# Optimization experiments

Measured on AMD Instinct MI355X. Metric: run time of the kernel, lower is better.

Reference implementation:

```python
import jax, jax.numpy as jnp
import numpy as np

D = 192
HEADS = 4
HD = D // HEADS
R = 3  # correlation radius actually used in forward_level
NDISP = (2 * R + 1) ** 2  # 49
T = 3  # frames -> 2 consecutive pairs
ITERS = 4


def layer_norm(x, w, b, eps=1e-5):
    m = jnp.mean(x, axis=-1, keepdims=True)
    v = jnp.var(x, axis=-1, keepdims=True)
    return (x - m) / jnp.sqrt(v + eps) * w + b


def mha(x, in_w, in_b, out_w, out_b):
    # torch nn.MultiheadAttention, batch_first, self-attention
    B, N, _ = x.shape
    qkv = x @ in_w.T + in_b
    q, k, v = jnp.split(qkv, 3, axis=-1)
    q = q.reshape(B, N, HEADS, HD).transpose(0, 2, 1, 3) * (1.0 / float(np.sqrt(HD)))
    k = k.reshape(B, N, HEADS, HD).transpose(0, 2, 1, 3)
    v = v.reshape(B, N, HEADS, HD).transpose(0, 2, 1, 3)
    att = jax.nn.softmax(jnp.einsum('bhqd,bhkd->bhqk', q, k), axis=-1)
    y = jnp.einsum('bhqk,bhkd->bhqd', att, v).transpose(0, 2, 1, 3).reshape(B, N, D)
    return y @ out_w.T + out_b


def tblock(x, p):
    ln1w, ln1b, inw, inb, ow, ob, ln2w, ln2b, w1, b1, w2, b2 = p
    x = x + mha(layer_norm(x, ln1w, ln1b), inw, inb, ow, ob)
    h = layer_norm(x, ln2w, ln2b)
    h = jax.nn.gelu(h @ w1.T + b1, approximate=False) @ w2.T + b2
    return x + h


def local_corr(f1, f2):
    C = f1.shape[1]
    scale = 1.0 / float(np.sqrt(C))
    outs = []
    for dy in range(-R, R + 1):
        for dx in range(-R, R + 1):
            f2s = jnp.roll(f2, (dy, dx), axis=(2, 3))
            outs.append(jnp.sum(f1 * f2s, axis=1) * scale)
    return jnp.stack(outs, axis=1)


def grid_sample_bilinear_border(img, grid):
    # img: B,C,H,W; grid: B,Ho,Wo,2 with (x,y) in [-1,1]; align_corners=True, border padding
    B, C, H, W = img.shape
    x = jnp.clip((grid[..., 0] + 1.0) * 0.5 * (W - 1), 0.0, W - 1)
    y = jnp.clip((grid[..., 1] + 1.0) * 0.5 * (H - 1), 0.0, H - 1)
    x0 = jnp.floor(x); y0 = jnp.floor(y)
    x1 = jnp.minimum(x0 + 1, W - 1); y1 = jnp.minimum(y0 + 1, H - 1)
    wx = (x - x0)[:, None]; wy = (y - y0)[:, None]
    imgf = img.reshape(B, C, H * W)
    Ho, Wo = x.shape[1], x.shape[2]
    def gather(yy, xx):
        idx = (yy * W + xx).astype(jnp.int32).reshape(B, 1, Ho * Wo)
        return jnp.take_along_axis(imgf, idx, axis=2).reshape(B, C, Ho, Wo)
    v00 = gather(y0, x0); v01 = gather(y0, x1)
    v10 = gather(y1, x0); v11 = gather(y1, x1)
    return v00 * (1 - wx) * (1 - wy) + v01 * wx * (1 - wy) + v10 * (1 - wx) * wy + v11 * wx * wy


def warp(img, flow):
    # flow in pixels, Bx2xHxW
    B, C, H, W = img.shape
    xs = jnp.linspace(-1.0, 1.0, W); ys = jnp.linspace(-1.0, 1.0, H)
    gx, gy = jnp.meshgrid(xs, ys)  # each (H, W), 'xy' indexing
    base = jnp.stack([gx, gy], axis=-1)[None]
    off = jnp.stack([flow[:, 0] * (2.0 / max(W - 1, 1)),
                     flow[:, 1] * (2.0 / max(H - 1, 1))], axis=-1)
    return grid_sample_bilinear_border(img, base + off)


def upsample2x_align(img):
    # F.interpolate(scale_factor=2, mode='bilinear', align_corners=True)
    B, C, H, W = img.shape
    Ho, Wo = 2 * H, 2 * W
    xs = jnp.linspace(-1.0, 1.0, Wo); ys = jnp.linspace(-1.0, 1.0, Ho)
    gx, gy = jnp.meshgrid(xs, ys)
    grid = jnp.broadcast_to(jnp.stack([gx, gy], axis=-1)[None], (B, Ho, Wo, 2))
    return grid_sample_bilinear_border(img, grid)


def conv2d(x, w, b):
    y = jax.lax.conv_general_dilated(x, w, (1, 1), ((1, 1), (1, 1)),
                                     dimension_numbers=('NCHW', 'OIHW', 'NCHW'))
    return y + b[None, :, None, None]


def _forward(feats_l1, feats_l2, feats_l3, tok_w, tok_b,
             lcm_ln1_w, lcm_ln1_b, lcm_in_w, lcm_in_b, lcm_out_w, lcm_out_b,
             lcm_ln2_w, lcm_ln2_b, lcm_mlp_w1, lcm_mlp_b1, lcm_mlp_w2, lcm_mlp_b2,
             gtr_ln1_w, gtr_ln1_b, gtr_in_w, gtr_in_b, gtr_out_w, gtr_out_b,
             gtr_ln2_w, gtr_ln2_b, gtr_mlp_w1, gtr_mlp_b1, gtr_mlp_w2, gtr_mlp_b2,
             head_w1, head_b1, head_w2, head_b2,
             ref1_w1, ref1_b1, ref1_w2, ref1_b2,
             ref0_w1, ref0_b1, ref0_w2, ref0_b2):
    feats = [[feats_l1[t] for t in range(T)],
             [feats_l2[t] for t in range(T)],
             [feats_l3[t] for t in range(T)]]
    # ---- CostTokenizer ----
    tokens = []
    for lvl in range(3):
        toks = []
        for k in range(T - 1):
            corr = local_corr(feats[lvl][k], feats[lvl][k + 1])
            toks.append(jnp.einsum('bchw,dc->bdhw', corr, tok_w[lvl]) + tok_b[lvl][None, :, None, None])
        tokens.append(toks)
    lcm_p = [(lcm_ln1_w[i], lcm_ln1_b[i], lcm_in_w[i], lcm_in_b[i], lcm_out_w[i], lcm_out_b[i],
              lcm_ln2_w[i], lcm_ln2_b[i], lcm_mlp_w1[i], lcm_mlp_b1[i], lcm_mlp_w2[i], lcm_mlp_b2[i])
             for i in range(lcm_ln1_w.shape[0])]
    gtr_p = [(gtr_ln1_w[i], gtr_ln1_b[i], gtr_in_w[i], gtr_in_b[i], gtr_out_w[i], gtr_out_b[i],
              gtr_ln2_w[i], gtr_ln2_b[i], gtr_mlp_w1[i], gtr_mlp_b1[i], gtr_mlp_w2[i], gtr_mlp_b2[i])
             for i in range(gtr_ln1_w.shape[0])]
    # ---- LatentCostMemory (EMA state; .detach() -> stop_gradient; state resets when N changes) ----
    state = None
    latent = []
    for toks in tokens:
        lvl_lat = []
        for tok in toks:
            B_, Dd, H, W = tok.shape
            x = tok.reshape(B_, Dd, H * W).transpose(0, 2, 1)  # b (h w) d
            for p in lcm_p:
                x = tblock(x, p)
            if state is None or state.shape[1] != x.shape[1]:
                state = jax.lax.stop_gradient(x)
            x = 0.8 * x + 0.2 * state
            state = jax.lax.stop_gradient(x)
            lvl_lat.append(x.transpose(0, 2, 1))  # b d n
        latent.append(lvl_lat)
    H8, W8 = feats[1][0].shape[-2:]
    coarse = []
    for lat in latent[1]:
        x = lat.transpose(0, 2, 1)
        for p in gtr_p:
            x = tblock(x, p)
        fv = jax.nn.gelu(x @ head_w1.T + head_b1, approximate=False) @ head_w2.T + head_b2
        coarse.append(fv.transpose(0, 2, 1).reshape(-1, 2, H8, W8))
    # ---- MSRecurrentDecoder ----
    outs = []
    for k, f8 in enumerate(coarse):
        cur = f8
        for _ in range(ITERS):
            w10 = warp(feats[1][k + 1], cur)
            x = jnp.concatenate([feats[1][k], cur, w10], axis=1)
            cur = cur + conv2d(jax.nn.gelu(conv2d(x, ref1_w1, ref1_b1), approximate=False), ref1_w2, ref1_b2)
        cur2 = upsample2x_align(cur)
        for _ in range(ITERS):
            w10 = warp(feats[0][k + 1], cur2)
            x = jnp.concatenate([feats[0][k], cur2, w10], axis=1)
            cur2 = cur2 + conv2d(jax.nn.gelu(conv2d(x, ref0_w1, ref0_b1), approximate=False), ref0_w2, ref0_b2)
        outs.append(cur2)
    return jnp.stack(outs)  # [pairs, B, 2, H/4, W/4]


def setup_inputs():
    key = jax.random.key(0)
    ks = iter(jax.random.split(key, 64))
    def rn(shape, s=1.0):
        return jax.random.normal(next(ks), shape, dtype=jnp.float32) * s
    B = 1
    inp = {}
    inp['feats_l1'] = rn((T, B, 64, 64, 64))
    inp['feats_l2'] = rn((T, B, 128, 32, 32))
    inp['feats_l3'] = rn((T, B, 192, 16, 16))
    inp['tok_w'] = rn((3, D, NDISP), 0.02)
    inp['tok_b'] = rn((3, D), 0.02)
    for pre, n in (('lcm', 6), ('gtr', 2)):
        inp[pre + '_ln1_w'] = jnp.ones((n, D), jnp.float32)
        inp[pre + '_ln1_b'] = jnp.zeros((n, D), jnp.float32)
        inp[pre + '_in_w'] = rn((n, 3 * D, D), 0.02)
        inp[pre + '_in_b'] = rn((n, 3 * D), 0.02)
        inp[pre + '_out_w'] = rn((n, D, D), 0.02)
        inp[pre + '_out_b'] = rn((n, D), 0.02)
        inp[pre + '_ln2_w'] = jnp.ones((n, D), jnp.float32)
        inp[pre + '_ln2_b'] = jnp.zeros((n, D), jnp.float32)
        inp[pre + '_mlp_w1'] = rn((n, 4 * D, D), 0.02)
        inp[pre + '_mlp_b1'] = rn((n, 4 * D), 0.02)
        inp[pre + '_mlp_w2'] = rn((n, D, 4 * D), 0.02)
        inp[pre + '_mlp_b2'] = rn((n, D), 0.02)
    inp['head_w1'] = rn((D, D), 0.02); inp['head_b1'] = rn((D,), 0.02)
    inp['head_w2'] = rn((2, D), 0.02); inp['head_b2'] = rn((2,), 0.02)
    inp['ref1_w1'] = rn((128, 258, 3, 3), 0.02); inp['ref1_b1'] = rn((128,), 0.02)
    inp['ref1_w2'] = rn((2, 128, 3, 3), 0.02); inp['ref1_b2'] = rn((2,), 0.02)
    inp['ref0_w1'] = rn((64, 130, 3, 3), 0.02); inp['ref0_b1'] = rn((64,), 0.02)
    inp['ref0_w2'] = rn((2, 64, 3, 3), 0.02); inp['ref0_b2'] = rn((2,), 0.02)
    return inp


def reference(feats_l1, feats_l2, feats_l3, tok_w, tok_b,
              lcm_ln1_w, lcm_ln1_b, lcm_in_w, lcm_in_b, lcm_out_w, lcm_out_b,
              lcm_ln2_w, lcm_ln2_b, lcm_mlp_w1, lcm_mlp_b1, lcm_mlp_w2, lcm_mlp_b2,
              gtr_ln1_w, gtr_ln1_b, gtr_in_w, gtr_in_b, gtr_out_w, gtr_out_b,
              gtr_ln2_w, gtr_ln2_b, gtr_mlp_w1, gtr_mlp_b1, gtr_mlp_w2, gtr_mlp_b2,
              head_w1, head_b1, head_w2, head_b2,
              ref1_w1, ref1_b1, ref1_w2, ref1_b2,
              ref0_w1, ref0_b1, ref0_w2, ref0_b2):
    return _forward(feats_l1, feats_l2, feats_l3, tok_w, tok_b,
                    lcm_ln1_w, lcm_ln1_b, lcm_in_w, lcm_in_b, lcm_out_w, lcm_out_b,
                    lcm_ln2_w, lcm_ln2_b, lcm_mlp_w1, lcm_mlp_b1, lcm_mlp_w2, lcm_mlp_b2,
                    gtr_ln1_w, gtr_ln1_b, gtr_in_w, gtr_in_b, gtr_out_w, gtr_out_b,
                    gtr_ln2_w, gtr_ln2_b, gtr_mlp_w1, gtr_mlp_b1, gtr_mlp_w2, gtr_mlp_b2,
                    head_w1, head_b1, head_w2, head_b2,
                    ref1_w1, ref1_b1, ref1_w2, ref1_b2,
                    ref0_w1, ref0_b1, ref0_w2, ref0_b2)
```

## Files before the change

kernel.cpp:

```cpp
#include <hip/hip_runtime.h>
#include <hip/hip_bf16.h>

typedef __hip_bfloat16 bf16;
typedef short bf16x8 __attribute__((ext_vector_type(8)));
typedef float f32x4 __attribute__((ext_vector_type(4)));

#define DEV __device__ __forceinline__

DEV float bf2f(bf16 v) { return __bfloat162float(v); }
DEV bf16 f2bf(float v) { return __float2bfloat16(v); }
DEV unsigned short bfr(float f) {
  bf16 h = __float2bfloat16(f);
  return *reinterpret_cast<unsigned short*>(&h);
}
DEV float shf(unsigned short u) {
  unsigned int x = ((unsigned int)u) << 16;
  return *reinterpret_cast<float*>(&x);
}
DEV float gelu_exact(float x) { return 0.5f * x * (1.0f + erff(x * 0.70710678118654752f)); }

DEV float ldw(const void* p, long i, int isb) {
  return isb ? __bfloat162float(((const bf16*)p)[i]) : ((const float*)p)[i];
}

__global__ void k_detect(const unsigned short* __restrict__ u, int* __restrict__ flag) {
  __shared__ int bad;
  if (threadIdx.x == 0) bad = 0;
  __syncthreads();
  for (int i = threadIdx.x; i < 8192; i += 256) {
    int expo = (u[i] >> 7) & 0xFF;
    if (expo >= 138) atomicOr(&bad, 1);
  }
  __syncthreads();
  if (threadIdx.x == 0) *flag = bad ? 0 : 1;
}
__global__ void k_setone(int* p) { *p = 1; }

__global__ void k_cvt(const void* __restrict__ s, float* __restrict__ d, int n,
                      const int* __restrict__ fl) {
  int isb = *fl;
  int i = blockIdx.x * blockDim.x + threadIdx.x;
  if (i < n) d[i] = ldw(s, i, isb);
}

__global__ void k_zerosh(unsigned short* __restrict__ p, int n8) {
  int i = blockIdx.x * blockDim.x + threadIdx.x;
  if (i < n8) { uint4 z = {0, 0, 0, 0}; *(uint4*)(p + (long)i * 8) = z; }
}

__global__ void k_padtokw(const void* __restrict__ tw, bf16* __restrict__ dst,
                          const int* __restrict__ fl) {
  int isb = *fl;
  int i = blockIdx.x * blockDim.x + threadIdx.x;
  if (i >= 12288) return;
  int n = i >> 6, k = i & 63;
  float v = (k < 49) ? ldw(tw, 9408 + (long)n * 49 + k, isb) : 0.0f;
  dst[i] = f2bf(v);
}

__global__ void k_packw(const void* __restrict__ src, bf16* __restrict__ dst,
                        int OC, int C, int ICT, int NP, int ICP, int n,
                        const int* __restrict__ fl) {
  int isb = *fl;
  int i = blockIdx.x * blockDim.x + threadIdx.x;
  if (i >= n) return;
  int s = i / (NP * ICP);
  int r = i - s * NP * ICP;
  int oc = r / ICP, icp = r - oc * ICP;
  float v = 0.0f;
  if (oc < OC) {
    int ic = -1;
    if (icp < C) ic = icp;
    else if (icp < 2 * C) ic = icp - C + C + 2;
    else if (icp < 2 * C + 2) ic = icp - 2 * C + C;
    if (ic >= 0 && ic < ICT) v = ldw(src, ((long)oc * ICT + ic) * 9 + s, isb);
  }
  dst[i] = f2bf(v);
}

__global__ void k_trans_feats(const void* __restrict__ in, bf16* __restrict__ Fp,
                              int F, int C, int HW, const int* __restrict__ fl) {
  int isb = *fl;
  int cpg = C >> 3;
  int n = F * HW * cpg;
  int i = blockIdx.x * blockDim.x + threadIdx.x;
  if (i >= n) return;
  int p = i % HW;
  int rem = i / HW;
  int c8 = rem % cpg;
  int f = rem / cpg;
  long base = (long)f * C * HW + (long)(c8 * 8) * HW + p;
  union { unsigned short u[8]; uint4 v; } pk;
#pragma unroll
  for (int j = 0; j < 8; ++j) pk.u[j] = bfr(ldw(in, base + (long)j * HW, isb));
  *(uint4*)((unsigned short*)Fp + ((long)f * HW + p) * C + c8 * 8) = pk.v;
}

template <int C, int ICP, int NP, int WW, int LGW>
__global__ __launch_bounds__(64) void k_conv1w(
    const bf16* __restrict__ Fp, const float* __restrict__ flow,
    const bf16* __restrict__ Wp, const float* __restrict__ bias,
    bf16* __restrict__ out) {
  constexpr int HH = WW, HW = WW * WW;
  constexpr int ACW = 18, APX = 54;
  constexpr int NK = ICP / 32;
  __shared__ unsigned short As[APX][40];
  __shared__ unsigned short Ws[144][40];
  __shared__ int pofs[APX];
  __shared__ int doff[APX][4];
  __shared__ float dwt[APX][4];
  __shared__ float ffl[APX][2];
  int ln = threadIdx.x;
  int quad = ln >> 4, l16 = ln & 15;
  int n0 = blockIdx.x * 16, m0 = blockIdx.y * 16, b = blockIdx.z;
  int py0 = m0 >> LGW, px0 = m0 & (WW - 1);
  const unsigned short* fcur = (const unsigned short*)Fp + (long)b * HW * C;
  const unsigned short* fnxt = (const unsigned short*)Fp + (long)(b + 1) * HW * C;
  const float* fl = flow + (long)b * 2 * HW;
  if (ln < APX) {
    int sr = ln / ACW, sc = ln - sr * ACW;
    int py = py0 + sr - 1, px = px0 + sc - 1;
    bool in = py >= 0 && py < HH && px >= 0 && px < WW;
    int p = in ? (py * WW + px) : 0;
    pofs[ln] = in ? p * C : -1;
    float fx = in ? fl[p] : 0.0f, fy = in ? fl[HW + p] : 0.0f;
    float x = fminf(fmaxf((float)px + fx, 0.0f), (float)(WW - 1));
    float y = fminf(fmaxf((float)py + fy, 0.0f), (float)(HH - 1));
    int x0 = (int)floorf(x), y0 = (int)floorf(y);
    int x1 = min(x0 + 1, WW - 1), y1 = min(y0 + 1, HH - 1);
    float wx = x - (float)x0, wy = y - (float)y0;
    dwt[ln][0] = in ? (1 - wx) * (1 - wy) : 0.0f;
    dwt[ln][1] = in ? wx * (1 - wy) : 0.0f;
    dwt[ln][2] = in ? (1 - wx) * wy : 0.0f;
    dwt[ln][3] = in ? wx * wy : 0.0f;
    doff[ln][0] = (y0 * WW + x0) * C; doff[ln][1] = (y0 * WW + x1) * C;
    doff[ln][2] = (y1 * WW + x0) * C; doff[ln][3] = (y1 * WW + x1) * C;
    ffl[ln][0] = in ? fx : 0.0f; ffl[ln][1] = in ? fy : 0.0f;
  }
  uint4 wrg[9];
  uint4 arg[4];
  uint4 qrg[4][4];
  auto ldW = [&](int kc) {
#pragma unroll
    for (int j = 0; j < 9; ++j) {
      int idx = ln + j * 64;
      int r = idx >> 2, c4 = idx & 3;
      int s = r >> 4, nl = r & 15;
      wrg[j] = *(const uint4*)((const unsigned short*)Wp +
               ((long)s * NP + n0 + nl) * ICP + kc * 32 + c4 * 8);
    }
  };
  auto stW = [&]() {
#pragma unroll
    for (int j = 0; j < 9; ++j) {
      int idx = ln + j * 64;
      int r = idx >> 2, c4 = idx & 3;
      *(uint4*)&Ws[r][c4 * 8] = wrg[j];
    }
  };
  auto ldA = [&](int kc) {
    int chb = kc * 32;
    if (chb < C) {
#pragma unroll
      for (int j = 0; j < 4; ++j) {
        int idx = ln + j * 64;
        if (idx < APX * 4) {
          int ap = idx >> 2, c4 = idx & 3;
          int po = pofs[ap];
          uint4 z = {0, 0, 0, 0};
          arg[j] = (po >= 0) ? *(const uint4*)(fcur + po + chb + c4 * 8) : z;
        }
      }
    } else if (chb < 2 * C) {
#pragma unroll
      for (int j = 0; j < 4; ++j) {
        int idx = ln + j * 64;
        if (idx < APX * 4) {
          int ap = idx >> 2, c4 = idx & 3;
          int c = chb - C + c4 * 8;
#pragma unroll
          for (int e = 0; e < 4; ++e)
            qrg[j][e] = *(const uint4*)(fnxt + doff[ap][e] + c);
        }
      }
    }
  };
  auto stA = [&](int kc) {
    int chb = kc * 32;
    if (chb < C) {
#pragma unroll
      for (int j = 0; j < 4; ++j) {
        int idx = ln + j * 64;
        if (idx < APX * 4) {
          int ap = idx >> 2, c4 = idx & 3;
          *(uint4*)&As[ap][c4 * 8] = arg[j];
        }
      }
    } else if (chb < 2 * C) {
#pragma unroll
      for (int j = 0; j < 4; ++j) {
        int idx = ln + j * 64;
        if (idx < APX * 4) {
          int ap = idx >> 2, c4 = idx & 3;
          union { unsigned short u[8]; uint4 v; } a0 = {.v = qrg[j][0]}, a1 = {.v = qrg[j][1]},
                                                  a2 = {.v = qrg[j][2]}, a3 = {.v = qrg[j][3]}, o;
          float q0 = dwt[ap][0], q1 = dwt[ap][1], q2 = dwt[ap][2], q3 = dwt[ap][3];
#pragma unroll
          for (int e = 0; e < 8; ++e)
            o.u[e] = bfr(shf(a0.u[e]) * q0 + shf(a1.u[e]) * q1 +
                         shf(a2.u[e]) * q2 + shf(a3.u[e]) * q3);
          *(uint4*)&As[ap][c4 * 8] = o.v;
        }
      }
    } else {
#pragma unroll
      for (int j = 0; j < 4; ++j) {
        int idx = ln + j * 64;
        if (idx < APX * 4) {
          int ap = idx >> 2, c4 = idx & 3;
          union { unsigned short u[8]; uint4 v; } o = { .v = {0, 0, 0, 0} };
          if (c4 == 0) { o.u[0] = bfr(ffl[ap][0]); o.u[1] = bfr(ffl[ap][1]); }
          *(uint4*)&As[ap][c4 * 8] = o.v;
        }
      }
    }
  };
  f32x4 ac0 = {}, ac1 = {}, ac2 = {};
  auto mm = [&]() {
#pragma unroll
    for (int s = 0; s < 9; ++s) {
      int ky = s / 3, kx = s - ky * 3;
      bf16x8 af = *(const bf16x8*)&As[ky * ACW + l16 + kx][quad * 8];
      bf16x8 wf = *(const bf16x8*)&Ws[s * 16 + l16][quad * 8];
      if (s % 3 == 0)      ac0 = __builtin_amdgcn_mfma_f32_16x16x32_bf16(af, wf, ac0, 0, 0, 0);
      else if (s % 3 == 1) ac1 = __builtin_amdgcn_mfma_f32_16x16x32_bf16(af, wf, ac1, 0, 0, 0);
      else                 ac2 = __builtin_amdgcn_mfma_f32_16x16x32_bf16(af, wf, ac2, 0, 0, 0);
    }
  };
  ldW(0); ldA(0);
  stW(); stA(0);
#pragma unroll
  for (int kc = 0; kc < NK; ++kc) {
    if (kc + 1 < NK) { ldW(kc + 1); ldA(kc + 1); }
    mm();
    if (kc + 1 < NK) { stW(); stA(kc + 1); }
  }
  int n = n0 + l16;
  float bv = bias[n];
  long rowbase = (long)b * (HH + 2) * (WW + 2) + (long)(py0 + 1) * (WW + 2);
#pragma unroll
  for (int r = 0; r < 4; ++r) {
    int px = px0 + quad * 4 + r;
    float v = gelu_exact(ac0[r] + ac1[r] + ac2[r] + bv);
    ((unsigned short*)out)[(rowbase + px + 1) * NP + n] = bfr(v);
  }
}

template <int C, int WW, int LGW>
__global__ __launch_bounds__(256) void k_conv2_dot(
    const bf16* __restrict__ mid, const bf16* __restrict__ Wq,
    const float* __restrict__ bias, float* __restrict__ cur) {
  constexpr int HH = WW;
  constexpr int HW = HH * WW;
  constexpr int Wp2 = WW + 2;
  constexpr int CPL = C / 64;
  int tid = threadIdx.x, wv = tid >> 6, ln = tid & 63;
  int gw = blockIdx.x * 4 + wv;
  int b = gw >> (2 * LGW);
  int p = gw & (HW - 1);
  int py = p >> LGW, px = p & (WW - 1);
  float r0 = cur[((long)b * 2 + 0) * HW + p];
  float r1 = cur[((long)b * 2 + 1) * HW + p];
  float b0 = bias[0], b1 = bias[1];
  const unsigned short* base = (const unsigned short*)mid +
      ((long)b * (HH + 2) * Wp2 + (long)py * Wp2 + px) * C + ln * CPL;
  const unsigned short* wb = (const unsigned short*)Wq + ln * CPL;
  float s0 = 0.0f, s1 = 0.0f;
#pragma unroll
  for (int t = 0; t < 9; ++t) {
    int dy = t / 3, dx = t - dy * 3;
    const unsigned short* ar = base + ((long)dy * Wp2 + dx) * C;
    const unsigned short* w0r = wb + (long)(t * 16 + 0) * C;
    const unsigned short* w1r = wb + (long)(t * 16 + 1) * C;
    if (CPL == 2) {
      unsigned int a = *(const unsigned int*)ar;
      unsigned int q0 = *(const unsigned int*)w0r;
      unsigned int q1 = *(const unsigned int*)w1r;
      float a0 = shf((unsigned short)a), a1 = shf((unsigned short)(a >> 16));
      s0 += a0 * shf((unsigned short)q0) + a1 * shf((unsigned short)(q0 >> 16));
      s1 += a0 * shf((unsigned short)q1) + a1 * shf((unsigned short)(q1 >> 16));
    } else {
      float a0 = shf(ar[0]);
      s0 += a0 * shf(w0r[0]);
      s1 += a0 * shf(w1r[0]);
    }
  }
#pragma unroll
  for (int o = 32; o; o >>= 1) { s0 += __shfl_xor(s0, o); s1 += __shfl_xor(s1, o); }
  if (ln == 0) {
    cur[((long)b * 2 + 0) * HW + p] = s0 + b0 + r0;
    cur[((long)b * 2 + 1) * HW + p] = s1 + b1 + r1;
  }
}

__global__ void k_corr(const bf16* __restrict__ Fp2, bf16* __restrict__ corrT) {
  __shared__ unsigned short f1r[128];
  int p = blockIdx.x;
  int b = blockIdx.y;
  int t = threadIdx.x;
  const unsigned short* f1 = (const unsigned short*)Fp2 + ((long)b * 1024 + p) * 128;
  if (t < 16) *(uint4*)&f1r[t * 8] = *(const uint4*)(f1 + t * 8);
  __syncthreads();
  long rowo = ((long)b * 1024 + p) * 64;
  if (t < 49) {
    int dy = t / 7 - 3, dx = t % 7 - 3;
    int h = p >> 5, w = p & 31;
    int p2 = (((h - dy) & 31) << 5) | ((w - dx) & 31);
    const unsigned short* f2 = (const unsigned short*)Fp2 + ((long)(b + 1) * 1024 + p2) * 128;
    float s = 0.0f;
    for (int c = 0; c < 128; c += 8) {
      union { unsigned short u[8]; uint4 v; } av = { .v = *(const uint4*)&f1r[c] };
      union { unsigned short u[8]; uint4 v; } bv = { .v = *(const uint4*)(f2 + c) };
#pragma unroll
      for (int j = 0; j < 8; ++j) s += shf(av.u[j]) * shf(bv.u[j]);
    }
    corrT[rowo + t] = f2bf(s * 0.08838834764831845f);
  } else {
    corrT[rowo + t] = f2bf(0.0f);
  }
}

template <int KT, int BM, int ACT, bool HASRES, int AMODE, int OUTBF, int VT>
__global__ __launch_bounds__(256) void k_gemm_mfma2(
    const void* __restrict__ A, const void* __restrict__ W, long woff,
    const void* __restrict__ bias, long boff, const int* __restrict__ flb,
    const float* __restrict__ res, void* __restrict__ C,
    int M, int N, const int* __restrict__ fl,
    const unsigned short* __restrict__ mop, const float* __restrict__ mml,
    bf16* __restrict__ vtout,
    const void* __restrict__ lnw, long lnwoff,
    const void* __restrict__ lnb, long lnboff) {
  (void)M;
  int isb = *fl;
  constexpr int NKC = ((KT < 192) ? KT : 192) >> 5;
  constexpr int WM = (BM == 64) ? 4 : 2;
  constexpr int NTW = (BM == 64) ? 4 : 2;
  constexpr int LPR = 256 / BM;
  constexpr int EPL = 192 / LPR;
  __shared__ unsigned short Asm[NKC][BM][40];
  __shared__ unsigned short Wsm[NKC][64][40];
  int tid = threadIdx.x;
  int wv = tid >> 6, ln = tid & 63;
  int quad = ln >> 4, l16 = ln & 15;
  int wm = wv % WM, wn = wv / WM;
  int m0 = blockIdx.y * BM, n0 = blockIdx.x * 64;
  f32x4 acc[NTW] = {};
  for (int s0 = 0; s0 < KT; s0 += 192) {
    if (s0) __syncthreads();
    for (int i = tid; i < NKC * 256; i += 256) {
      int c4 = i & 3, r = (i >> 2) & 63, kc = i >> 8;
      long eo = woff + (long)(n0 + r) * KT + s0 + kc * 32 + c4 * 8;
      if (isb) {
        *(uint4*)&Wsm[kc][r][c4 * 8] = *(const uint4*)((const unsigned short*)W + eo);
      } else {
        const float* wp = (const float*)W + eo;
        float4 w0 = *(const float4*)wp;
        float4 w1 = *(const float4*)(wp + 4);
        union { unsigned short u[8]; uint4 v; } pk;
        pk.u[0] = bfr(w0.x); pk.u[1] = bfr(w0.y); pk.u[2] = bfr(w0.z); pk.u[3] = bfr(w0.w);
        pk.u[4] = bfr(w1.x); pk.u[5] = bfr(w1.y); pk.u[6] = bfr(w1.z); pk.u[7] = bfr(w1.w);
        *(uint4*)&Wsm[kc][r][c4 * 8] = pk.v;
      }
    }
    if constexpr (AMODE == 1) {
      for (int i = tid; i < NKC * BM * 4; i += 256) {
        int c4 = i & 3, r = (i >> 2) % BM, kc = i / (BM * 4);
        const unsigned short* ap =
            (const unsigned short*)A + (long)(m0 + r) * KT + s0 + kc * 32 + c4 * 8;
        *(uint4*)&Asm[kc][r][c4 * 8] = *(const uint4*)ap;
      }
    } else if constexpr (AMODE == 0) {
      for (int i = tid; i < NKC * BM * 4; i += 256) {
        int c4 = i & 3, r = (i >> 2) % BM, kc = i / (BM * 4);
        const float* ap = (const float*)A + (long)(m0 + r) * KT + s0 + kc * 32 + c4 * 8;
        float4 a0 = *(const float4*)ap;
        float4 a1 = *(const float4*)(ap + 4);
        union { unsigned short u[8]; uint4 v; } pk;
        pk.u[0] = bfr(a0.x); pk.u[1] = bfr(a0.y); pk.u[2] = bfr(a0.z); pk.u[3] = bfr(a0.w);
        pk.u[4] = bfr(a1.x); pk.u[5] = bfr(a1.y); pk.u[6] = bfr(a1.z); pk.u[7] = bfr(a1.w);
        *(uint4*)&Asm[kc][r][c4 * 8] = pk.v;
      }
    } else if constexpr (AMODE == 3) {
      int row = tid / LPR, j = tid % LPR;
      const float* xr = (const float*)A + (long)(m0 + row) * 192 + j * EPL;
      float av[EPL];
#pragma unroll
      for (int q4 = 0; q4 < EPL / 4; ++q4) {
        float4 v = *(const float4*)(xr + q4 * 4);
        av[q4 * 4 + 0] = v.x; av[q4 * 4 + 1] = v.y;
        av[q4 * 4 + 2] = v.z; av[q4 * 4 + 3] = v.w;
      }
      float sum = 0.0f;
#pragma unroll
      for (int q = 0; q < EPL; ++q) sum += av[q];
#pragma unroll
      for (int o = 1; o < LPR; o <<= 1) sum += __shfl_xor(sum, o);
      float mean = sum * (1.0f / 192.0f);
      float vs = 0.0f;
#pragma unroll
      for (int q = 0; q < EPL; ++q) { float d = av[q] - mean; vs += d * d; }
#pragma unroll
      for (int o = 1; o < LPR; o <<= 1) vs += __shfl_xor(vs, o);
      float rstd = rsqrtf(vs * (1.0f / 192.0f) + 1e-5f);
#pragma unroll
      for (int g = 0; g < EPL / 8; ++g) {
        int k = j * EPL + g * 8;
        union { unsigned short u[8]; uint4 v; } pk;
#pragma unroll
        for (int e = 0; e < 8; ++e) {
          float gg = ldw(lnw, lnwoff + k + e, isb);
          float bb = ldw(lnb, lnboff + k + e, isb);
          pk.u[e] = bfr((av[g * 8 + e] - mean) * rstd * gg + bb);
        }
        *(uint4*)&Asm[k >> 5][row][k & 31] = pk.v;
      }
    } else {
      int row = tid / LPR, j = tid % LPR;
      int m = m0 + row;
      int rr = m & 1023, bb = m >> 10;
#pragma unroll
      for (int g = 0; g < EPL / 8; ++g) {
        int k = j * EPL + g * 8;
        int h = k / 48;
        int d0 = k - h * 48;
        long idx[4];
        float ms[4], ls[4];
        float Ms = -1e30f;
#pragma unroll
        for (int s = 0; s < 4; ++s) {
          idx[s] = (((long)s * 2 + bb) * 4 + h) * 1024 + rr;
          ms[s] = mml[idx[s] * 2];
          ls[s] = mml[idx[s] * 2 + 1];
          Ms = fmaxf(Ms, ms[s]);
        }
        float e[4], L = 0.0f;
#pragma unroll
        for (int s = 0; s < 4; ++s) { e[s] = __expf(ms[s] - Ms); L += ls[s] * e[s]; }
        float invL = 1.0f / L;
        union { unsigned short u[8]; uint4 v; } pk;
#pragma unroll
        for (int e2 = 0; e2 < 8; ++e2) {
          float o = 0.0f;
#pragma unroll
          for (int s = 0; s < 4; ++s) o += shf(mop[idx[s] * 48 + d0 + e2]) * e[s];
          pk.u[e2] = bfr(o * invL);
        }
        *(uint4*)&Asm[k >> 5][row][k & 31] = pk.v;
      }
    }
    __syncthreads();
#pragma unroll
    for (int kc = 0; kc < NKC; ++kc) {
      bf16x8 af = *(const bf16x8*)&Asm[kc][wm * 16 + l16][quad * 8];
#pragma unroll
      for (int nt = 0; nt < NTW; ++nt) {
        bf16x8 wf = *(const bf16x8*)&Wsm[kc][(wn * NTW + nt) * 16 + l16][quad * 8];
        acc[nt] = __builtin_amdgcn_mfma_f32_16x16x32_bf16(af, wf, acc[nt], 0, 0, 0);
      }
    }
  }
  int isbb = *flb;
#pragma unroll
  for (int nt = 0; nt < NTW; ++nt) {
    int n = n0 + (wn * NTW + nt) * 16 + l16;
    float bv = ldw(bias, boff + n, isbb);
#pragma unroll
    for (int r = 0; r < 4; ++r) {
      int m = m0 + wm * 16 + quad * 4 + r;
      float v = acc[nt][r] + bv;
      if (HASRES) v += res[(long)m * N + n];
      if (ACT == 1) v = gelu_exact(v);
      if (OUTBF) ((bf16*)C)[(long)m * N + n] = f2bf(v);
      else ((float*)C)[(long)m * N + n] = v;
      if constexpr (VT) {
        if (n >= 384) {
          int hh = (n - 384) / 48, dd = (n - 384) % 48;
          int row = m & 1023, bb = m >> 10;
          vtout[((long)(bb * 4 + hh) * 48 + dd) * 1024 + row] = f2bf(v);
        }
      }
    }
  }
}

__global__ __launch_bounds__(256) void k_head2(const float* __restrict__ A,
                                               const void* __restrict__ W,
                                               const void* __restrict__ bias,
                                               float* __restrict__ C,
                                               const int* __restrict__ fl) {
  int isb = *fl;
  int wv = threadIdx.x >> 6, ln = threadIdx.x & 63;
  int gw = blockIdx.x * 4 + wv;
  int m = gw >> 1, n = gw & 1;
  const float* a = A + (long)m * 192;
  float s = 0.0f;
#pragma unroll
  for (int q = 0; q < 3; ++q) {
    int j = ln + q * 64;
    s += a[j] * ldw(W, (long)n * 192 + j, isb);
  }
  for (int o = 32; o; o >>= 1) s += __shfl_xor(s, o);
  if (ln == 0) {
    int b = m >> 10, p = m & 1023;
    C[((long)b * 2 + n) * 1024 + p] = s + ldw(bias, n, isb);
  }
}

__global__ __launch_bounds__(256) void k_attn_mfma(const bf16* __restrict__ qkv,
                                                   const bf16* __restrict__ vt,
                                                   unsigned short* __restrict__ opart,
                                                   float* __restrict__ ml) {
  __shared__ unsigned short Qs[64][72];
  __shared__ unsigned short Ks[64][72];
  __shared__ unsigned short Vs[48][72];
  __shared__ unsigned short Ps[64][72];
  int tid = threadIdx.x;
  int wv = tid >> 6, ln = tid & 63, quad = ln >> 4, l16 = ln & 15;
  int h = blockIdx.y, b = blockIdx.z;
  int qt = blockIdx.x >> 2, s = blockIdx.x & 3;
  int q0 = qt * 64;
  const unsigned short* qp = (const unsigned short*)qkv + (long)b * 1024 * 576;
  const unsigned short* vp = (const unsigned short*)vt + ((long)(b * 4 + h) * 48) * 1024;
  for (int i = tid; i < 384; i += 256) {
    int r = i / 6, c = i % 6;
    *(uint4*)&Qs[r][c * 8] = *(const uint4*)(qp + (long)(q0 + r) * 576 + h * 48 + c * 8);
  }
  for (int i = tid; i < 128; i += 256) {
    int r = i >> 1, c = 6 + (i & 1);
    uint4 z = {0, 0, 0, 0};
    *(uint4*)&Qs[r][c * 8] = z;
  }
  float m[4] = {-1e30f, -1e30f, -1e30f, -1e30f};
  float l[4] = {0.0f, 0.0f, 0.0f, 0.0f};
  f32x4 accO[3] = {};
  const float SC = 0.14433756729740643f;
  for (int kc = s * 4; kc < s * 4 + 4; ++kc) {
    int k0 = kc * 64;
    for (int i = tid; i < 384; i += 256) {
      int r = i / 6, c = i % 6;
      *(uint4*)&Ks[r][c * 8] = *(const uint4*)(qp + (long)(k0 + r) * 576 + 192 + h * 48 + c * 8);
    }
    for (int i = tid; i < 128; i += 256) {
      int r = i >> 1, c = 6 + (i & 1);
      uint4 z = {0, 0, 0, 0};
      *(uint4*)&Ks[r][c * 8] = z;
    }
    for (int i = tid; i < 384; i += 256) {
      int d = i >> 3, c = i & 7;
      *(uint4*)&Vs[d][c * 8] = *(const uint4*)(vp + (long)d * 1024 + k0 + c * 8);
    }
    __syncthreads();
    f32x4 accS[4] = {};
    bf16x8 a0 = *(const bf16x8*)&Qs[wv * 16 + l16][quad * 8];
    bf16x8 a1 = *(const bf16x8*)&Qs[wv * 16 + l16][32 + quad * 8];
#pragma unroll
    for (int ct = 0; ct < 4; ++ct) {
      bf16x8 b0 = *(const bf16x8*)&Ks[ct * 16 + l16][quad * 8];
      bf16x8 b1 = *(const bf16x8*)&Ks[ct * 16 + l16][32 + quad * 8];
      accS[ct] = __builtin_amdgcn_mfma_f32_16x16x32_bf16(a0, b0, accS[ct], 0, 0, 0);
      accS[ct] = __builtin_amdgcn_mfma_f32_16x16x32_bf16(a1, b1, accS[ct], 0, 0, 0);
    }
#pragma unroll
    for (int r = 0; r < 4; ++r) {
      float s0 = accS[0][r] * SC, s1 = accS[1][r] * SC;
      float s2 = accS[2][r] * SC, s3 = accS[3][r] * SC;
      float mx = fmaxf(fmaxf(s0, s1), fmaxf(s2, s3));
      for (int o = 8; o; o >>= 1) mx = fmaxf(mx, __shfl_xor(mx, o));
      float mn = fmaxf(m[r], mx);
      float alpha = __expf(m[r] - mn);
      float p0 = __expf(s0 - mn), p1 = __expf(s1 - mn);
      float p2 = __expf(s2 - mn), p3 = __expf(s3 - mn);
      float rs = p0 + p1 + p2 + p3;
      for (int o = 8; o; o >>= 1) rs += __shfl_xor(rs, o);
      m[r] = mn;
      l[r] = l[r] * alpha + rs;
      accO[0][r] *= alpha; accO[1][r] *= alpha; accO[2][r] *= alpha;
      int prow = wv * 16 + quad * 4 + r;
      Ps[prow][l16]      = bfr(p0);
      Ps[prow][16 + l16] = bfr(p1);
      Ps[prow][32 + l16] = bfr(p2);
      Ps[prow][48 + l16] = bfr(p3);
    }
    bf16x8 pf0 = *(const bf16x8*)&Ps[wv * 16 + l16][quad * 8];
    bf16x8 pf1 = *(const bf16x8*)&Ps[wv * 16 + l16][32 + quad * 8];
#pragma unroll
    for (int ct = 0; ct < 3; ++ct) {
      bf16x8 v0 = *(const bf16x8*)&Vs[ct * 16 + l16][quad * 8];
      bf16x8 v1 = *(const bf16x8*)&Vs[ct * 16 + l16][32 + quad * 8];
      accO[ct] = __builtin_amdgcn_mfma_f32_16x16x32_bf16(pf0, v0, accO[ct], 0, 0, 0);
      accO[ct] = __builtin_amdgcn_mfma_f32_16x16x32_bf16(pf1, v1, accO[ct], 0, 0, 0);
    }
    __syncthreads();
  }
  long base = (((long)s * 2 + b) * 4 + h) * 1024;
#pragma unroll
  for (int r = 0; r < 4; ++r) {
    int row = q0 + wv * 16 + quad * 4 + r;
#pragma unroll
    for (int ct = 0; ct < 3; ++ct)
      opart[(base + row) * 48 + ct * 16 + l16] = bfr(accO[ct][r]);
    if (l16 == 0) {
      ml[(base + row) * 2]     = m[r];
      ml[(base + row) * 2 + 1] = l[r];
    }
  }
}

__global__ void k_ema(float* __restrict__ x) {
  int i = blockIdx.x * blockDim.x + threadIdx.x;
  if (i < 196608) x[196608 + i] = 0.8f * x[196608 + i] + 0.2f * x[i];
}

__global__ void k_upsample(const float* __restrict__ in, float* __restrict__ out) {
  int i = blockIdx.x * blockDim.x + threadIdx.x;
  if (i >= 2 * 2 * 64 * 64) return;
  int p = i & 4095;
  int bc = i >> 12;
  int oy = p >> 6, ox = p & 63;
  float sx = ox * (31.0f / 63.0f), sy = oy * (31.0f / 63.0f);
  int x0 = (int)sx, y0 = (int)sy;
  int x1 = min(x0 + 1, 31), y1 = min(y0 + 1, 31);
  float wx = sx - x0, wy = sy - y0;
  const float* ic = in + (long)bc * 1024;
  out[i] = ic[y0 * 32 + x0] * (1 - wx) * (1 - wy) + ic[y0 * 32 + x1] * wx * (1 - wy)
         + ic[y1 * 32 + x0] * (1 - wx) * wy      + ic[y1 * 32 + x1] * wx * wy;
}

__global__ void k_out(const float* __restrict__ cur2, void* __restrict__ out,
                      const int* __restrict__ fl) {
  int isb = *fl;
  int i = blockIdx.x * blockDim.x + threadIdx.x;
  if (i < 16384) {
    if (isb) ((bf16*)out)[i] = f2bf(cur2[i]);
    else ((float*)out)[i] = cur2[i];
  }
}

extern "C" void kernel_launch(void* const* d_in, const int* in_sizes, int n_in,
                              void* d_out, int out_size, void* d_ws, size_t ws_size,
                              hipStream_t stream) {
  const void* feats_l1 = d_in[0];
  const void* feats_l2 = d_in[1];
  const void* tok_w = d_in[3];
  const void* tok_b = d_in[4];
  const void* lcm_ln1_w = d_in[5];
  const void* lcm_ln1_b = d_in[6];
  const void* lcm_in_w  = d_in[7];
  const void* lcm_in_b  = d_in[8];
  const void* lcm_out_w = d_in[9];
  const void* lcm_out_b = d_in[10];
  const void* lcm_ln2_w = d_in[11];
  const void* lcm_ln2_b = d_in[12];
  const void* lcm_mlp_w1 = d_in[13];
  const void* lcm_mlp_b1 = d_in[14];
  const void* lcm_mlp_w2 = d_in[15];
  const void* lcm_mlp_b2 = d_in[16];
  const void* gtr_ln1_w = d_in[17];
  const void* gtr_ln1_b = d_in[18];
  const void* gtr_in_w  = d_in[19];
  const void* gtr_in_b  = d_in[20];
  const void* gtr_out_w = d_in[21];
  const void* gtr_out_b = d_in[22];
  const void* gtr_ln2_w = d_in[23];
  const void* gtr_ln2_b = d_in[24];
  const void* gtr_mlp_w1 = d_in[25];
  const void* gtr_mlp_b1 = d_in[26];
  const void* gtr_mlp_w2 = d_in[27];
  const void* gtr_mlp_b2 = d_in[28];
  const void* head_w1 = d_in[29];
  const void* head_b1 = d_in[30];
  const void* head_w2 = d_in[31];
  const void* head_b2 = d_in[32];
  const void* ref1_w1 = d_in[33];
  const void* ref1_b1 = d_in[34];
  const void* ref1_w2 = d_in[35];
  const void* ref1_b2 = d_in[36];
  const void* ref0_w1 = d_in[37];
  const void* ref0_b1 = d_in[38];
  const void* ref0_w2 = d_in[39];
  const void* ref0_b2 = d_in[40];
  (void)ws_size; (void)n_in; (void)in_sizes; (void)out_size;

  int* flag = (int*)d_ws;
  int* oneflag = (int*)d_ws + 2;
  float* wsf = (float*)d_ws;
  float* F2   = wsf + 16;
  float* rA   = F2 + 393216;
  float* rX   = rA + 786432;
  float* rT   = rX + 393216;
  float* rY   = rT + 393216;
  float* big  = rY + 393216;
  float* fv   = big + 1572864;
  float* cur  = fv + 4096;
  float* cur2 = cur + 4096;
  float* cb1a = cur2 + 16384;
  float* cb1b = cb1a + 128;
  float* cb0a = cb1b + 16;
  float* cb0b = cb0a + 64;
  bf16* wtok  = (bf16*)(cb0b + 16);
  float* wpk  = cb0b + 16 + 6144;
  bf16* w1p1 = (bf16*)wpk;
  bf16* w1p2 = (bf16*)(wpk + 165888);
  bf16* w0p1 = (bf16*)(wpk + 175104);
  bf16* w0p2 = (bf16*)(wpk + 221184);

  float* x = rX;
  bf16* corrTb = (bf16*)big;
  bf16* qkvbb  = (bf16*)big;
  bf16* vtb    = (bf16*)(big + 655360);
  bf16* hidb   = (bf16*)big;
  unsigned short* opart = (unsigned short*)rA;
  float* mlbuf = rY;
  float* headh = rT;
  bf16* mid0p = (bf16*)rT;
  bf16* mid1p = (bf16*)rY;
  bf16* Fp2   = (bf16*)(big + 851968);
  bf16* Fp1   = (bf16*)(big + 1048576);

  k_detect<<<1, 256, 0, stream>>>((const unsigned short*)feats_l1, flag);
  k_setone<<<1, 1, 0, stream>>>(oneflag);
  k_cvt<<<1, 256, 0, stream>>>(ref1_b1, cb1a, 128, flag);
  k_cvt<<<1, 256, 0, stream>>>(ref1_b2, cb1b, 2, flag);
  k_cvt<<<1, 256, 0, stream>>>(ref0_b1, cb0a, 64, flag);
  k_cvt<<<1, 256, 0, stream>>>(ref0_b2, cb0b, 2, flag);
  k_padtokw<<<48, 256, 0, stream>>>(tok_w, wtok, flag);
  k_packw<<<1296, 256, 0, stream>>>(ref1_w1, w1p1, 128, 128, 258, 128, 288, 331776, flag);
  k_packw<<<72, 256, 0, stream>>>(ref1_w2, w1p2, 2, 128, 128, 16, 128, 18432, flag);
  k_packw<<<360, 256, 0, stream>>>(ref0_w1, w0p1, 64, 64, 130, 64, 160, 92160, flag);
  k_packw<<<36, 256, 0, stream>>>(ref0_w2, w0p2, 2, 64, 64, 16, 64, 9216, flag);
  k_trans_feats<<<192, 256, 0, stream>>>(feats_l2, Fp2, 3, 128, 1024, flag);
  k_trans_feats<<<384, 256, 0, stream>>>(feats_l1, Fp1, 3, 64, 4096, flag);

  k_corr<<<dim3(1024, 2), 64, 0, stream>>>(Fp2, corrTb);
  k_gemm_mfma2<64, 32, 0, false, 1, 0, 0><<<dim3(3, 64), 256, 0, stream>>>(
      corrTb, wtok, 0, tok_b, 192, flag, nullptr, x, 2048, 192, oneflag,
      nullptr, nullptr, nullptr, nullptr, 0, nullptr, 0);

  auto run_block = [&](const void* ln1w, long o1, const void* ln1b, long o2,
                       const void* inw, long o3, const void* inb, long o4,
                       const void* ow, long o5, const void* ob, long o6,
                       const void* ln2w, long o7, const void* ln2b, long o8,
                       const void* w1, long o9, const void* b1, long o10,
                       const void* w2, long o11, const void* b2, long o12) {
    k_gemm_mfma2<192, 64, 0, false, 3, 1, 1><<<dim3(9, 32), 256, 0, stream>>>(
        x, inw, o3, inb, o4, flag, nullptr, qkvbb, 2048, 576, flag,
        nullptr, nullptr, vtb, ln1w, o1, ln1b, o2);
    k_attn_mfma<<<dim3(64, 4, 2), 256, 0, stream>>>(qkvbb, vtb, opart, mlbuf);
    k_gemm_mfma2<192, 32, 0, true, 2, 0, 0><<<dim3(3, 64), 256, 0, stream>>>(
        nullptr, ow, o5, ob, o6, flag, x, x, 2048, 192, flag,
        opart, mlbuf, nullptr, nullptr, 0, nullptr, 0);
    k_gemm_mfma2<192, 64, 1, false, 3, 1, 0><<<dim3(12, 32), 256, 0, stream>>>(
        x, w1, o9, b1, o10, flag, nullptr, hidb, 2048, 768, flag,
        nullptr, nullptr, nullptr, ln2w, o7, ln2b, o8);
    k_gemm_mfma2<768, 32, 0, true, 1, 0, 0><<<dim3(3, 64), 256, 0, stream>>>(
        hidb, w2, o11, b2, o12, flag, x, x, 2048, 192, flag,
        nullptr, nullptr, nullptr, nullptr, 0, nullptr, 0);
  };

  for (int i = 0; i < 6; ++i) {
    run_block(lcm_ln1_w, (long)i * 192, lcm_ln1_b, (long)i * 192,
              lcm_in_w, (long)i * 110592, lcm_in_b, (long)i * 576,
              lcm_out_w, (long)i * 36864, lcm_out_b, (long)i * 192,
              lcm_ln2_w, (long)i * 192, lcm_ln2_b, (long)i * 192,
              lcm_mlp_w1, (long)i * 147456, lcm_mlp_b1, (long)i * 768,
              lcm_mlp_w2, (long)i * 147456, lcm_mlp_b2, (long)i * 192);
  }
  k_ema<<<768, 256, 0, stream>>>(x);

  for (int i = 0; i < 2; ++i) {
    run_block(gtr_ln1_w, (long)i * 192, gtr_ln1_b, (long)i * 192,
              gtr_in_w, (long)i * 110592, gtr_in_b, (long)i * 576,
              gtr_out_w, (long)i * 36864, gtr_out_b, (long)i * 192,
              gtr_ln2_w, (long)i * 192, gtr_ln2_b, (long)i * 192,
              gtr_mlp_w1, (long)i * 147456, gtr_mlp_b1, (long)i * 768,
              gtr_mlp_w2, (long)i * 147456, gtr_mlp_b2, (long)i * 192);
  }

  k_gemm_mfma2<192, 32, 1, false, 0, 0, 0><<<dim3(3, 64), 256, 0, stream>>>(
      x, head_w1, 0, head_b1, 0, flag, nullptr, headh, 2048, 192, flag,
      nullptr, nullptr, nullptr, nullptr, 0, nullptr, 0);
  k_head2<<<1024, 256, 0, stream>>>(headh, head_w2, head_b2, cur, flag);

  k_zerosh<<<768, 256, 0, stream>>>((unsigned short*)rT, 196608);

  for (int it = 0; it < 4; ++it) {
    k_conv1w<128, 288, 128, 32, 5><<<dim3(8, 64, 2), 64, 0, stream>>>(
        Fp2, cur, w1p1, cb1a, mid1p);
    k_conv2_dot<128, 32, 5><<<512, 256, 0, stream>>>(mid1p, w1p2, cb1b, cur);
  }
  k_upsample<<<64, 256, 0, stream>>>(cur, cur2);

  for (int it = 0; it < 4; ++it) {
    k_conv1w<64, 160, 64, 64, 6><<<dim3(4, 256, 2), 64, 0, stream>>>(
        Fp1, cur2, w0p1, cb0a, mid0p);
    k_conv2_dot<64, 64, 6><<<2048, 256, 0, stream>>>(mid0p, w0p2, cb0b, cur2);
  }

  k_out<<<64, 256, 0, stream>>>(cur2, d_out, flag);
}
```

Before: 1.106 ms.

## Read conv weights directly from global and drop LDS staging and prefetch

Restructures the warped 3x3 conv kernel. MFMA weight fragments are now read straight from global memory instead of being staged through an LDS tile, and the register double-buffered prefetch of the next K-chunk is removed in favour of a simple load, store, multiply loop. A launch bound asking for two blocks per CU is added. The aim is to cut LDS footprint and register pressure so more waves fit per CU. In exchange, global load latency is no longer overlapped with MFMA work, and weight reads rely on cache hits.

```diff
diff --git a/kernel.cpp b/kernel.cpp
--- a/kernel.cpp
+++ b/kernel.cpp
@@ -97,7 +97,7 @@
 }
 
 template <int C, int ICP, int NP, int WW, int LGW>
-__global__ __launch_bounds__(64) void k_conv1w(
+__global__ __launch_bounds__(64, 2) void k_conv1d(
     const bf16* __restrict__ Fp, const float* __restrict__ flow,
     const bf16* __restrict__ Wp, const float* __restrict__ bias,
     bf16* __restrict__ out) {
@@ -105,7 +105,6 @@
   constexpr int ACW = 18, APX = 54;
   constexpr int NK = ICP / 32;
   __shared__ unsigned short As[APX][40];
-  __shared__ unsigned short Ws[144][40];
   __shared__ int pofs[APX];
   __shared__ int doff[APX][4];
   __shared__ float dwt[APX][4];
@@ -137,30 +136,12 @@
     doff[ln][2] = (y1 * WW + x0) * C; doff[ln][3] = (y1 * WW + x1) * C;
     ffl[ln][0] = in ? fx : 0.0f; ffl[ln][1] = in ? fy : 0.0f;
   }
-  uint4 wrg[9];
-  uint4 arg[4];
-  uint4 qrg[4][4];
-  auto ldW = [&](int kc) {
-#pragma unroll
-    for (int j = 0; j < 9; ++j) {
-      int idx = ln + j * 64;
-      int r = idx >> 2, c4 = idx & 3;
-      int s = r >> 4, nl = r & 15;
-      wrg[j] = *(const uint4*)((const unsigned short*)Wp +
-               ((long)s * NP + n0 + nl) * ICP + kc * 32 + c4 * 8);
-    }
-  };
-  auto stW = [&]() {
-#pragma unroll
-    for (int j = 0; j < 9; ++j) {
-      int idx = ln + j * 64;
-      int r = idx >> 2, c4 = idx & 3;
-      *(uint4*)&Ws[r][c4 * 8] = wrg[j];
-    }
-  };
-  auto ldA = [&](int kc) {
+  const unsigned short* wrow = (const unsigned short*)Wp + (long)(n0 + l16) * ICP + quad * 8;
+  f32x4 ac0 = {}, ac1 = {}, ac2 = {};
+  for (int kc = 0; kc < NK; ++kc) {
     int chb = kc * 32;
     if (chb < C) {
+      uint4 arg[4];
 #pragma unroll
       for (int j = 0; j < 4; ++j) {
         int idx = ln + j * 64;
@@ -171,23 +152,6 @@
           arg[j] = (po >= 0) ? *(const uint4*)(fcur + po + chb + c4 * 8) : z;
         }
       }
-    } else if (chb < 2 * C) {
-#pragma unroll
-      for (int j = 0; j < 4; ++j) {
-        int idx = ln + j * 64;
-        if (idx < APX * 4) {
-          int ap = idx >> 2, c4 = idx & 3;
-          int c = chb - C + c4 * 8;
-#pragma unroll
-          for (int e = 0; e < 4; ++e)
-            qrg[j][e] = *(const uint4*)(fnxt + doff[ap][e] + c);
-        }
-      }
-    }
-  };
-  auto stA = [&](int kc) {
-    int chb = kc * 32;
-    if (chb < C) {
 #pragma unroll
       for (int j = 0; j < 4; ++j) {
         int idx = ln + j * 64;
@@ -202,9 +166,14 @@
         int idx = ln + j * 64;
         if (idx < APX * 4) {
           int ap = idx >> 2, c4 = idx & 3;
-          union { unsigned short u[8]; uint4 v; } a0 = {.v = qrg[j][0]}, a1 = {.v = qrg[j][1]},
-                                                  a2 = {.v = qrg[j][2]}, a3 = {.v = qrg[j][3]}, o;
+          int c = chb - C + c4 * 8;
+          uint4 v0 = *(const uint4*)(fnxt + doff[ap][0] + c);
+          uint4 v1 = *(const uint4*)(fnxt + doff[ap][1] + c);
+          uint4 v2 = *(const uint4*)(fnxt + doff[ap][2] + c);
+          uint4 v3 = *(const uint4*)(fnxt + doff[ap][3] + c);
           float q0 = dwt[ap][0], q1 = dwt[ap][1], q2 = dwt[ap][2], q3 = dwt[ap][3];
+          union { unsigned short u[8]; uint4 v; } a0 = {.v = v0}, a1 = {.v = v1},
+                                                  a2 = {.v = v2}, a3 = {.v = v3}, o;
 #pragma unroll
           for (int e = 0; e < 8; ++e)
             o.u[e] = bfr(shf(a0.u[e]) * q0 + shf(a1.u[e]) * q1 +
@@ -224,26 +193,15 @@
         }
       }
     }
-  };
-  f32x4 ac0 = {}, ac1 = {}, ac2 = {};
-  auto mm = [&]() {
 #pragma unroll
     for (int s = 0; s < 9; ++s) {
       int ky = s / 3, kx = s - ky * 3;
       bf16x8 af = *(const bf16x8*)&As[ky * ACW + l16 + kx][quad * 8];
-      bf16x8 wf = *(const bf16x8*)&Ws[s * 16 + l16][quad * 8];
+      bf16x8 wf = *(const bf16x8*)(wrow + (long)s * NP * ICP + chb);
       if (s % 3 == 0)      ac0 = __builtin_amdgcn_mfma_f32_16x16x32_bf16(af, wf, ac0, 0, 0, 0);
       else if (s % 3 == 1) ac1 = __builtin_amdgcn_mfma_f32_16x16x32_bf16(af, wf, ac1, 0, 0, 0);
       else                 ac2 = __builtin_amdgcn_mfma_f32_16x16x32_bf16(af, wf, ac2, 0, 0, 0);
     }
-  };
-  ldW(0); ldA(0);
-  stW(); stA(0);
-#pragma unroll
-  for (int kc = 0; kc < NK; ++kc) {
-    if (kc + 1 < NK) { ldW(kc + 1); ldA(kc + 1); }
-    mm();
-    if (kc + 1 < NK) { stW(); stA(kc + 1); }
   }
   int n = n0 + l16;
   float bv = bias[n];
@@ -794,14 +752,14 @@
   k_zerosh<<<768, 256, 0, stream>>>((unsigned short*)rT, 196608);
 
   for (int it = 0; it < 4; ++it) {
-    k_conv1w<128, 288, 128, 32, 5><<<dim3(8, 64, 2), 64, 0, stream>>>(
+    k_conv1d<128, 288, 128, 32, 5><<<dim3(8, 64, 2), 64, 0, stream>>>(
         Fp2, cur, w1p1, cb1a, mid1p);
     k_conv2_dot<128, 32, 5><<<512, 256, 0, stream>>>(mid1p, w1p2, cb1b, cur);
   }
   k_upsample<<<64, 256, 0, stream>>>(cur, cur2);
 
   for (int it = 0; it < 4; ++it) {
-    k_conv1w<64, 160, 64, 64, 6><<<dim3(4, 256, 2), 64, 0, stream>>>(
+    k_conv1d<64, 160, 64, 64, 6><<<dim3(4, 256, 2), 64, 0, stream>>>(
         Fp1, cur2, w0p1, cb0a, mid0p);
     k_conv2_dot<64, 64, 6><<<2048, 256, 0, stream>>>(mid0p, w0p2, cb0b, cur2);
   }
```

Result: faster. 994.5 us (-10.1%).
